# Performance work log

Measured on AMD Instinct MI355X. Metric: run time of the kernel, lower is better.

## Reference

```python
import jax, jax.numpy as jnp
import numpy as np
from jax import lax

DN = ('NCHW', 'OIHW', 'NCHW')


def squash(x):
    # x: [..., d]; squared-norm over last dim
    sq = jnp.sum(x * x, axis=-1, keepdims=True)
    return sq * x / ((1.0 + sq) * jnp.sqrt(sq))


def setup_inputs() -> dict:
    key = jax.random.key(0)
    ks = jax.random.split(key, 6)
    B = 512
    x = jax.random.normal(ks[0], (B, 1, 28, 28), dtype=jnp.float32)
    conv1_w = jax.random.normal(ks[1], (256, 1, 9, 9), dtype=jnp.float32) * 0.05
    conv1_b = jnp.zeros((256,), dtype=jnp.float32)
    conv2_w = jax.random.normal(ks[2], (256, 256, 9, 9), dtype=jnp.float32) * 0.02
    conv2_b = jnp.zeros((256,), dtype=jnp.float32)
    # W: [num_routes=1152, num_capsules=10, out_channels=16, in_channels=8]
    W = jax.random.normal(ks[3], (1152, 10, 16, 8), dtype=jnp.float32)
    return {"x": x, "conv1_w": conv1_w, "conv1_b": conv1_b,
            "conv2_w": conv2_w, "conv2_b": conv2_b, "W": W}


def reference(x, conv1_w, conv1_b, conv2_w, conv2_b, W):
    B = x.shape[0]
    # conv1 + ReLU: [B,1,28,28] -> [B,256,20,20]
    h = lax.conv_general_dilated(x, conv1_w, (1, 1), 'VALID', dimension_numbers=DN)
    h = jax.nn.relu(h + conv1_b[None, :, None, None])
    # primary capsule conv: [B,256,20,20] -> [B,256,6,6], stride 2
    h = lax.conv_general_dilated(h, conv2_w, (2, 2), 'VALID', dimension_numbers=DN)
    h = h + conv2_b[None, :, None, None]
    # reshape to capsules [B, 1152, 8] (matches torch .view on NCHW) and squash
    u = squash(h.reshape(B, -1, 8))
    # u_hat[b,r,c,o] = W[r,c,o,i] @ u[b,r,i]
    u_hat = jnp.einsum('rcoi,bri->brco', W, u)  # [B,1152,10,16]
    R, C = W.shape[0], W.shape[1]
    b_ij = jnp.zeros((R, C), dtype=x.dtype)
    num_iterations = 3
    for it in range(num_iterations):
        c_ij = jax.nn.softmax(b_ij, axis=0)          # softmax over routes
        s_j = jnp.einsum('rc,brco->bco', c_ij, u_hat)  # [B,10,16]
        v_j = squash(s_j)
        if it < num_iterations - 1:
            a_ij = jnp.einsum('brco,bco->brc', u_hat, v_j)  # agreement
            b_ij = b_ij + a_ij.mean(axis=0)
    return v_j  # [B,10,16]
```

## Files before the change

### kernel.cpp

```cpp
#include <hip/hip_runtime.h>
#include <stdint.h>


typedef unsigned short u16;
typedef unsigned int u32;
typedef _Float16 half8 __attribute__((ext_vector_type(8)));
typedef float f32x4 __attribute__((ext_vector_type(4)));

__device__ __forceinline__ u16 f2h(float f) {
  union { _Float16 h; u16 u; } cv;
  cv.h = (_Float16)f;
  return cv.u;
}

__device__ __forceinline__ void gload_lds16(const void* g, void* l) {
  __builtin_amdgcn_global_load_lds(
      (const __attribute__((address_space(1))) void*)g,
      (__attribute__((address_space(3))) void*)l, 16, 0, 0);
}

__global__ __launch_bounds__(256) void prologue_kernel(
    const float* __restrict__ x, const float* __restrict__ w1,
    const float* __restrict__ b1, const float* __restrict__ w2,
    const float* __restrict__ b2, u16* __restrict__ hT,
    u16* __restrict__ A2, float* __restrict__ u) {
  __shared__ __align__(16) char smraw[81 * 264 * 2];
  int bid = blockIdx.x;
  int tid = threadIdx.x;
  if (bid < 512) {
    float* xs = (float*)smraw;
    int b = bid;
    int co = tid;
    for (int i = co; i < 784; i += 256) xs[i] = x[(size_t)b * 784 + i];
    float w[81];
    const float* wp = w1 + co * 81;
#pragma unroll
    for (int k = 0; k < 81; ++k) w[k] = wp[k];
    float bias = b1[co];
    __syncthreads();
    u16* hb = hT + (size_t)b * 102400 + co;
    for (int yp = 0; yp < 10; ++yp) {
      int y0 = yp * 2;
      for (int g = 0; g < 5; ++g) {
        int xo = g * 4;
        float a0[4], a1[4];
#pragma unroll
        for (int j = 0; j < 4; ++j) { a0[j] = bias; a1[j] = bias; }
#pragma unroll
        for (int ky2 = 0; ky2 < 10; ++ky2) {
          const float* row = &xs[(y0 + ky2) * 28 + xo];
          float4 r0 = *(const float4*)row;
          float4 r1 = *(const float4*)(row + 4);
          float4 r2 = *(const float4*)(row + 8);
          float xr[12] = {r0.x, r0.y, r0.z, r0.w, r1.x, r1.y, r1.z, r1.w,
                          r2.x, r2.y, r2.z, r2.w};
          if (ky2 < 9) {
#pragma unroll
            for (int kx = 0; kx < 9; ++kx) {
              float wv = w[ky2 * 9 + kx];
              a0[0] = fmaf(wv, xr[kx], a0[0]);
              a0[1] = fmaf(wv, xr[kx + 1], a0[1]);
              a0[2] = fmaf(wv, xr[kx + 2], a0[2]);
              a0[3] = fmaf(wv, xr[kx + 3], a0[3]);
            }
          }
          if (ky2 >= 1) {
#pragma unroll
            for (int kx = 0; kx < 9; ++kx) {
              float wv = w[(ky2 - 1) * 9 + kx];
              a1[0] = fmaf(wv, xr[kx], a1[0]);
              a1[1] = fmaf(wv, xr[kx + 1], a1[1]);
              a1[2] = fmaf(wv, xr[kx + 2], a1[2]);
              a1[3] = fmaf(wv, xr[kx + 3], a1[3]);
            }
          }
        }
#pragma unroll
        for (int j = 0; j < 4; ++j) {
          hb[(y0 * 20 + xo + j) * 256] = f2h(fmaxf(a0[j], 0.f));
          hb[((y0 + 1) * 20 + xo + j) * 256] = f2h(fmaxf(a1[j], 0.f));
        }
      }
    }
  } else if (bid < 768) {
    u16* tl = (u16*)smraw;
    int co = bid - 512;
    const float* wp = w2 + (size_t)co * 20736;
#pragma unroll
    for (int k = 0; k < 81; ++k) {
      int li = k * 256 + tid;
      int ci = li / 81, t = li - ci * 81;
      tl[t * 264 + ci] = f2h(wp[li]);
    }
    __syncthreads();
    u16* op = A2 + (size_t)co * 20736;
    for (int oc = tid; oc < 2592; oc += 256) {
      int k0 = oc * 8;
      int t = k0 >> 8, ci0 = k0 & 255;
      *(uint4*)(op + k0) = *(const uint4*)&tl[t * 264 + ci0];
    }
  } else {
    int i = (bid - 768) * 256 + tid;
    int b = i / 2304, j0 = (i - b * 2304) * 4;
    float4 v;
    v.x = b2[j0 / 36]; v.y = b2[(j0 + 1) / 36];
    v.z = b2[(j0 + 2) / 36]; v.w = b2[(j0 + 3) / 36];
    *(float4*)(u + (size_t)b * 9216 + j0) = v;
  }
}

__global__ __launch_bounds__(512, 2) void conv2_kernel(
    const u16* __restrict__ hT, const u16* __restrict__ A2,
    float* __restrict__ u) {
  __shared__ __align__(16) u16 lds_[65536];
  char* const ldsc = (char*)lds_;
  const int bx = blockIdx.x;
  const int nbk = bx % 72, kz = bx / 72;
  const int n0 = nbk * 256;
  const int tid = threadIdx.x;
  const int lane = tid & 63, w = tid >> 6;
  const int wr = w >> 2, wc = w & 3;
  const int fr = lane & 15, fg = lane >> 4;
  const int w1024 = w * 1024;

  const int rA = tid >> 3;
  const int qsrc = (tid & 7) ^ (rA & 7);
  const int AbaseT = rA * 20736 + qsrc * 8;
  int Bb[4];
#pragma unroll
  for (int rg = 0; rg < 4; ++rg) {
    int n = n0 + rg * 64 + rA;
    int b = n / 36, sp = n - b * 36, oh = sp / 6, ow = sp - oh * 6;
    Bb[rg] = (b * 400 + oh * 40 + ow * 2) * 256 + qsrc * 8;
  }

  const int kx0 = (fg ^ (fr & 7)) << 4;
  const int kx1 = ((4 + fg) ^ (fr & 7)) << 4;
  const int wr16384 = wr * 16384;
  const int bh16384 = 32768 + (wc >> 1) * 16384;
  const int brow0 = (wc & 1) * 64;

  f32x4 acc[8][4] = {};
  half8 areg[4][2], breg[2][2];

#define STAGE_A(E, H, GT) do {                                               \
    char* p_ = ldsc + (E) * 65536 + (H) * 16384 + w1024;                     \
    gload_lds16(A2 + AbaseT + ((H) * 2 + 0) * 1327104 + (GT) * 64, p_);      \
    gload_lds16(A2 + AbaseT + ((H) * 2 + 1) * 1327104 + (GT) * 64, p_ + 8192); \
  } while (0)
#define STAGE_B(E, H, BOFF) do {                                             \
    char* p_ = ldsc + (E) * 65536 + 32768 + (H) * 16384 + w1024;             \
    gload_lds16(hT + Bb[(H) * 2 + 0] + (BOFF), p_);                          \
    gload_lds16(hT + Bb[(H) * 2 + 1] + (BOFF), p_ + 8192);                   \
  } while (0)
#define STAGE_ALL(E, GT) do {                                                \
    int tap_ = (GT) >> 2;                                                    \
    int kh_ = tap_ / 9, kw_ = tap_ - kh_ * 9;                                \
    int bo_ = (kh_ * 20 + kw_) * 256 + ((GT) & 3) * 64;                      \
    STAGE_A(E, 0, GT); STAGE_B(E, 0, bo_);                                   \
    STAGE_B(E, 1, bo_); STAGE_A(E, 1, GT);                                   \
  } while (0)
#define RD_A(D, MH) do { _Pragma("unroll")                                   \
    for (int mr = 0; mr < 4; ++mr) {                                         \
      const char* r_ = ldsc + (D) * 65536 + wr16384 +                        \
                       ((MH) * 64 + mr * 16 + fr) * 128;                     \
      areg[mr][0] = *(const half8*)(r_ + kx0);                               \
      areg[mr][1] = *(const half8*)(r_ + kx1);                               \
    } } while (0)
#define RD_B(D, NH) do { _Pragma("unroll")                                   \
    for (int nr = 0; nr < 2; ++nr) {                                         \
      const char* r_ = ldsc + (D) * 65536 + bh16384 +                        \
                       (brow0 + (NH) * 32 + nr * 16 + fr) * 128;             \
      breg[nr][0] = *(const half8*)(r_ + kx0);                               \
      breg[nr][1] = *(const half8*)(r_ + kx1);                               \
    } } while (0)
#define MM16(MH, NH) do {                                                    \
    __builtin_amdgcn_s_setprio(1);                                           \
    _Pragma("unroll") for (int mr = 0; mr < 4; ++mr)                         \
    _Pragma("unroll") for (int nr = 0; nr < 2; ++nr) {                       \
      acc[(MH)*4+mr][(NH)*2+nr] = __builtin_amdgcn_mfma_f32_16x16x32_f16(    \
          areg[mr][0], breg[nr][0], acc[(MH)*4+mr][(NH)*2+nr], 0, 0, 0);     \
      acc[(MH)*4+mr][(NH)*2+nr] = __builtin_amdgcn_mfma_f32_16x16x32_f16(    \
          areg[mr][1], breg[nr][1], acc[(MH)*4+mr][(NH)*2+nr], 0, 0, 0);     \
    }                                                                        \
    __builtin_amdgcn_s_setprio(0);                                           \
  } while (0)
#define BAR_PRE() do {                                                       \
    __builtin_amdgcn_s_barrier();                                            \
    asm volatile("s_waitcnt lgkmcnt(0)" ::: "memory");                       \
    __builtin_amdgcn_sched_barrier(0);                                       \
  } while (0)
#define BAR_ONLY() do {                                                      \
    __builtin_amdgcn_s_barrier();                                            \
    asm volatile("" ::: "memory");                                           \
  } while (0)
#define VM_BAR(N) do {                                                       \
    asm volatile("s_waitcnt vmcnt(" N ")" ::: "memory");                     \
    __builtin_amdgcn_s_barrier();                                            \
    asm volatile("" ::: "memory");                                           \
  } while (0)
#define TILE_STD(T, D, E) do {                                               \
    RD_A(D, 0); RD_B(D, 0);                                                  \
    STAGE_ALL(E, kz * 108 + (T) + 1);                                        \
    BAR_PRE(); MM16(0, 0); BAR_ONLY();                                       \
    RD_B(D, 1);                                                              \
    BAR_PRE(); MM16(0, 1); VM_BAR("8");                                      \
    RD_A(D, 1);                                                              \
    BAR_PRE(); MM16(1, 1); BAR_ONLY();                                       \
    RD_B(D, 0);                                                              \
    BAR_PRE(); MM16(1, 0); VM_BAR("2");                                      \
  } while (0)
#define TILE_LAST(D) do {                                                    \
    RD_A(D, 0); RD_B(D, 0);                                                  \
    BAR_PRE(); MM16(0, 0); BAR_ONLY();                                       \
    RD_B(D, 1);                                                              \
    BAR_PRE(); MM16(0, 1); VM_BAR("0");                                      \
    RD_A(D, 1);                                                              \
    BAR_PRE(); MM16(1, 1); BAR_ONLY();                                       \
    RD_B(D, 0);                                                              \
    BAR_PRE(); MM16(1, 0);                                                   \
  } while (0)

  STAGE_ALL(0, kz * 108);
  asm volatile("s_waitcnt vmcnt(2)" ::: "memory");
  __builtin_amdgcn_s_barrier();
  asm volatile("" ::: "memory");

  for (int tt = 0; tt < 53; ++tt) {
    TILE_STD(2 * tt, 0, 1);
    TILE_STD(2 * tt + 1, 1, 0);
  }
  TILE_STD(106, 0, 1);
  TILE_LAST(1);

#pragma unroll
  for (int nf = 0; nf < 4; ++nf) {
    int cn = n0 + wc * 64 + nf * 16 + fr;
    int ob = cn / 36;
    int os = cn - ob * 36;
    float* op = u + (size_t)ob * 9216 + os;
#pragma unroll
    for (int mf = 0; mf < 8; ++mf) {
      int row0 = wr * 128 + mf * 16 + fg * 4;
#pragma unroll
      for (int qq = 0; qq < 4; ++qq)
        atomicAdd(op + (row0 + qq) * 36, acc[mf][nf][qq]);
    }
  }
#undef STAGE_A
#undef STAGE_B
#undef STAGE_ALL
#undef RD_A
#undef RD_B
#undef MM16
#undef BAR_PRE
#undef BAR_ONLY
#undef VM_BAR
#undef TILE_STD
#undef TILE_LAST
}

__global__ __launch_bounds__(256) void squash_kernel(
    float* __restrict__ u, u16* __restrict__ ub) {
  int idx = blockIdx.x * 256 + threadIdx.x;
  float* up = u + (size_t)idx * 8;
  float4 a = *(const float4*)up;
  float4 c = *(const float4*)(up + 4);
  float sq = a.x * a.x + a.y * a.y + a.z * a.z + a.w * a.w +
             c.x * c.x + c.y * c.y + c.z * c.z + c.w * c.w;
  float f = sqrtf(sq) / (1.0f + sq);
  a.x *= f; a.y *= f; a.z *= f; a.w *= f;
  c.x *= f; c.y *= f; c.z *= f; c.w *= f;
  *(float4*)up = a;
  *(float4*)(up + 4) = c;
  u16 o[8];
  o[0] = f2h(a.x); o[1] = f2h(a.y); o[2] = f2h(a.z); o[3] = f2h(a.w);
  o[4] = f2h(c.x); o[5] = f2h(c.y); o[6] = f2h(c.z); o[7] = f2h(c.w);
  *(uint4*)(ub + (size_t)idx * 8) = *(uint4*)o;
}

__global__ __launch_bounds__(256) void transp_kernel(
    const u16* __restrict__ ub, u16* __restrict__ ubT) {
  __shared__ u16 tl[64][72];
  int ri0 = blockIdx.x * 64, b0 = blockIdx.y * 64;
  int tid = threadIdx.x;
  int br = tid >> 2, cq = tid & 3;
  const u16* ip = ub + (size_t)(b0 + br) * 9216 + ri0 + cq * 16;
  uint4 v0 = *(const uint4*)ip;
  uint4 v1 = *(const uint4*)(ip + 8);
  *(uint4*)&tl[br][cq * 16] = v0;
  *(uint4*)&tl[br][cq * 16 + 8] = v1;
  __syncthreads();
  int rr = tid >> 2, cb = tid & 3;
  u16 o0[8], o1[8];
#pragma unroll
  for (int j = 0; j < 8; ++j) {
    o0[j] = tl[cb * 16 + j][rr];
    o1[j] = tl[cb * 16 + 8 + j][rr];
  }
  u16* opp = ubT + (size_t)(ri0 + rr) * 512 + b0 + cb * 16;
  *(uint4*)opp = *(uint4*)o0;
  *(uint4*)(opp + 8) = *(uint4*)o1;
}

__global__ __launch_bounds__(256) void softmax_c_kernel(
    const float* __restrict__ bij, float* __restrict__ cT) {
  int c = blockIdx.x;
  int tid = threadIdx.x;
  __shared__ float red[256];
  float mx = -1e30f;
  for (int r = tid; r < 1152; r += 256) mx = fmaxf(mx, bij[r * 10 + c]);
  red[tid] = mx;
  __syncthreads();
  for (int s = 128; s > 0; s >>= 1) {
    if (tid < s) red[tid] = fmaxf(red[tid], red[tid + s]);
    __syncthreads();
  }
  mx = red[0];
  __syncthreads();
  float sum = 0.f;
  for (int r = tid; r < 1152; r += 256) sum += expf(bij[r * 10 + c] - mx);
  red[tid] = sum;
  __syncthreads();
  for (int s = 128; s > 0; s >>= 1) {
    if (tid < s) red[tid] += red[tid + s];
    __syncthreads();
  }
  float inv = 1.0f / red[0];
  for (int r = tid; r < 1152; r += 256)
    cT[c * 1152 + r] = expf(bij[r * 10 + c] - mx) * inv;
}

__global__ __launch_bounds__(256) void gemm_s_kernel(
    const float* __restrict__ W, const float* __restrict__ cT,
    const u16* __restrict__ ub, float* __restrict__ s) {
  __shared__ __align__(16) u16 Asl[160 * 72];
  __shared__ __align__(16) u16 Bsl[64 * 72];
  int nb = blockIdx.x & 7, kzi = blockIdx.x >> 3;
  int n0 = nb * 64, k0 = kzi * 256;
  int tid = threadIdx.x;
  int lane = tid & 63, wave = tid >> 6;
  int fr = lane & 15, fg = lane >> 4;

  f32x4 acc[10] = {};
#pragma unroll
  for (int st = 0; st < 4; ++st) {
    int kb = k0 + st * 64;
    __syncthreads();
#pragma unroll
    for (int j = 0; j < 5; ++j) {
      int c5 = tid + j * 256;
      int row = c5 >> 3, qq = c5 & 7;
      int cls = row >> 4, o = row & 15;
      int r = (kb + qq * 8) >> 3;
      const float* wp = W + (size_t)r * 1280 + cls * 128 + o * 8;
      float4 w0 = *(const float4*)wp;
      float4 w1 = *(const float4*)(wp + 4);
      float cs = cT[cls * 1152 + r] * 512.0f;
      u16 ov[8];
      ov[0] = f2h(w0.x * cs); ov[1] = f2h(w0.y * cs);
      ov[2] = f2h(w0.z * cs); ov[3] = f2h(w0.w * cs);
      ov[4] = f2h(w1.x * cs); ov[5] = f2h(w1.y * cs);
      ov[6] = f2h(w1.z * cs); ov[7] = f2h(w1.w * cs);
      *(uint4*)((char*)Asl + row * 144 + qq * 16) = *(uint4*)ov;
    }
#pragma unroll
    for (int j = 0; j < 2; ++j) {
      int c2 = tid + j * 256;
      int row = c2 >> 3, qq = c2 & 7;
      *(uint4*)((char*)Bsl + row * 144 + qq * 16) =
          *(const uint4*)(ub + (size_t)(n0 + row) * 9216 + kb + qq * 8);
    }
    __syncthreads();
#pragma unroll
    for (int s2 = 0; s2 < 2; ++s2) {
      int xg = (s2 * 4 + fg) * 16;
      half8 bf0 = *(const half8*)((char*)Bsl + (wave * 16 + fr) * 144 + xg);
#pragma unroll
      for (int m = 0; m < 10; ++m) {
        half8 af = *(const half8*)((char*)Asl + (m * 16 + fr) * 144 + xg);
        acc[m] = __builtin_amdgcn_mfma_f32_16x16x32_f16(af, bf0, acc[m], 0, 0, 0);
      }
    }
  }
  int bcol = n0 + wave * 16 + fr;
#pragma unroll
  for (int m = 0; m < 10; ++m)
#pragma unroll
    for (int qq = 0; qq < 4; ++qq)
      atomicAdd(s + (m * 16 + fg * 4 + qq) * 512 + bcol, acc[m][qq]);
}

__global__ __launch_bounds__(256) void squash_v_kernel(
    float* __restrict__ s, u16* __restrict__ vb) {
  int idx = blockIdx.x * 256 + threadIdx.x;
  int c = idx >> 9, b = idx & 511;
  float vals[16];
  float sq = 0.f;
#pragma unroll
  for (int o = 0; o < 16; ++o) {
    float v = s[(c * 16 + o) * 512 + b] * (1.0f / 512.0f);
    vals[o] = v;
    sq += v * v;
  }
#pragma unroll
  for (int o = 0; o < 16; ++o) s[(c * 16 + o) * 512 + b] = 0.f;
  float f = sqrtf(sq) / (1.0f + sq);
#pragma unroll
  for (int o = 0; o < 16; ++o)
    vb[(c * 16 + o) * 512 + b] = f2h(vals[o] * f * 4096.0f);
}

__global__ __launch_bounds__(256) void gemm_gc_kernel(
    const u16* __restrict__ vb, const u16* __restrict__ ubT,
    const float* __restrict__ W, float* __restrict__ bij) {
  __shared__ __align__(16) u16 Agl[160 * 72];
  __shared__ __align__(16) u16 Bgl[128 * 72];
  __shared__ float Gl[160 * 129];
  int nb = blockIdx.x % 72, kzi = blockIdx.x / 72;
  int n0 = nb * 128, k0 = kzi * 128;
  int tid = threadIdx.x;
  int lane = tid & 63, wave = tid >> 6;
  int fr = lane & 15, fg = lane >> 4;
  f32x4 acc[10][2] = {};
#pragma unroll
  for (int st = 0; st < 2; ++st) {
    int kb = k0 + st * 64;
    __syncthreads();
#pragma unroll
    for (int j = 0; j < 5; ++j) {
      int c5 = tid + j * 256;
      int row = c5 >> 3, qq = c5 & 7;
      *(uint4*)((char*)Agl + row * 144 + qq * 16) =
          *(const uint4*)(vb + (size_t)row * 512 + kb + qq * 8);
    }
#pragma unroll
    for (int j = 0; j < 4; ++j) {
      int c4 = tid + j * 256;
      int row = c4 >> 3, qq = c4 & 7;
      *(uint4*)((char*)Bgl + row * 144 + qq * 16) =
          *(const uint4*)(ubT + (size_t)(n0 + row) * 512 + kb + qq * 8);
    }
    __syncthreads();
#pragma unroll
    for (int s2 = 0; s2 < 2; ++s2) {
      int xg = (s2 * 4 + fg) * 16;
      half8 bfv[2];
#pragma unroll
      for (int nn = 0; nn < 2; ++nn)
        bfv[nn] = *(const half8*)((char*)Bgl + (wave * 32 + nn * 16 + fr) * 144 + xg);
#pragma unroll
      for (int m = 0; m < 10; ++m) {
        half8 af = *(const half8*)((char*)Agl + (m * 16 + fr) * 144 + xg);
#pragma unroll
        for (int nn = 0; nn < 2; ++nn)
          acc[m][nn] = __builtin_amdgcn_mfma_f32_16x16x32_f16(af, bfv[nn],
                                                             acc[m][nn], 0, 0, 0);
      }
    }
  }
#pragma unroll
  for (int m = 0; m < 10; ++m)
#pragma unroll
    for (int nn = 0; nn < 2; ++nn) {
      int col = wave * 32 + nn * 16 + fr;
#pragma unroll
      for (int qq = 0; qq < 4; ++qq)
        Gl[(m * 16 + fg * 4 + qq) * 129 + col] = acc[m][nn][qq];
    }
  __syncthreads();
  if (tid < 160) {
    int rl = tid / 10, c = tid - rl * 10;
    int r = (n0 >> 3) + rl;
    const float* wp = W + (size_t)r * 1280 + c * 128;
    float a = 0.f;
#pragma unroll 4
    for (int o = 0; o < 16; ++o) {
      const float* gp = &Gl[(c * 16 + o) * 129 + rl * 8];
#pragma unroll
      for (int i = 0; i < 8; ++i) a = fmaf(wp[o * 8 + i], gp[i], a);
    }
    atomicAdd(&bij[r * 10 + c], a * (1.0f / (512.0f * 4096.0f)));
  }
}

__global__ __launch_bounds__(256) void route_final_kernel(
    const float* __restrict__ cT, const float* __restrict__ u,
    const float* __restrict__ W, float* __restrict__ outp) {
  int c = blockIdx.y, b0 = blockIdx.x * 16;
  int tid = threadIdx.x, lb = tid >> 4, o = tid & 15;
  __shared__ float us[16][32][8];
  __shared__ float Wl[32][128];
  __shared__ float cs[32];
  float acc = 0.f;
  for (int r0 = 0; r0 < 1152; r0 += 32) {
    __syncthreads();
#pragma unroll
    for (int j = 0; j < 4; ++j) {
      int i4 = tid + j * 256;
      int bb = i4 >> 6, rem = i4 & 63;
      int rr = rem >> 1, hf = rem & 1;
      *(float4*)&us[bb][rr][hf * 4] =
          *(const float4*)&u[(size_t)(b0 + bb) * 9216 + (r0 + rr) * 8 + hf * 4];
    }
#pragma unroll
    for (int j = 0; j < 4; ++j) {
      int i4 = tid + j * 256;
      int rw = i4 >> 5, c4 = i4 & 31;
      *(float4*)&Wl[rw][c4 * 4] =
          *(const float4*)&W[((size_t)(r0 + rw) * 10 + c) * 128 + c4 * 4];
    }
    if (tid < 32) cs[tid] = cT[c * 1152 + r0 + tid];
    __syncthreads();
#pragma unroll 4
    for (int rr = 0; rr < 32; ++rr) {
      float4 w0 = *(const float4*)&Wl[rr][o * 8];
      float4 w1v = *(const float4*)&Wl[rr][o * 8 + 4];
      float4 ua = *(const float4*)&us[lb][rr][0];
      float4 ub4 = *(const float4*)&us[lb][rr][4];
      float d = w0.x * ua.x + w0.y * ua.y + w0.z * ua.z + w0.w * ua.w +
                w1v.x * ub4.x + w1v.y * ub4.y + w1v.z * ub4.z + w1v.w * ub4.w;
      acc = fmaf(cs[rr], d, acc);
    }
  }
  float sq = acc * acc;
  sq += __shfl_xor(sq, 1, 64);
  sq += __shfl_xor(sq, 2, 64);
  sq += __shfl_xor(sq, 4, 64);
  sq += __shfl_xor(sq, 8, 64);
  float f = sqrtf(sq) / (1.0f + sq);
  outp[((size_t)(b0 + lb) * 10 + c) * 16 + o] = acc * f;
}

extern "C" void kernel_launch(void* const* d_in, const int* in_sizes, int n_in,
                              void* d_out, int out_size, void* d_ws, size_t ws_size,
                              hipStream_t stream) {
  const float* x  = (const float*)d_in[0];
  const float* w1 = (const float*)d_in[1];
  const float* b1 = (const float*)d_in[2];
  const float* w2 = (const float*)d_in[3];
  const float* b2 = (const float*)d_in[4];
  const float* W  = (const float*)d_in[5];
  char* ws = (char*)d_ws;
  u16*   hT  = (u16*)ws;
  u16*   A2  = (u16*)(ws + 104857600);
  float* u   = (float*)(ws + 115474432);
  float* bij = (float*)(ws + 134348800);
  float* cT  = (float*)(ws + 134394880);
  float* s   = (float*)(ws + 134440960);
  u16*   ub  = (u16*)ws;
  u16*   ubT = (u16*)(ws + 9437184);
  u16*   vb  = (u16*)(ws + 21823488);
  float* out = (float*)d_out;

  hipMemsetAsync(bij, 0, 46080, stream);
  hipMemsetAsync(s, 0, 327680, stream);
  prologue_kernel<<<5376, 256, 0, stream>>>(x, w1, b1, w2, b2, hT, A2, u);
  conv2_kernel<<<216, 512, 0, stream>>>(hT, A2, u);
  squash_kernel<<<2304, 256, 0, stream>>>(u, ub);
  transp_kernel<<<dim3(144, 8), 256, 0, stream>>>(ub, ubT);
  for (int it = 0; it < 3; ++it) {
    softmax_c_kernel<<<10, 256, 0, stream>>>(bij, cT);
    if (it < 2) {
      gemm_s_kernel<<<288, 256, 0, stream>>>(W, cT, ub, s);
      squash_v_kernel<<<20, 256, 0, stream>>>(s, vb);
      gemm_gc_kernel<<<288, 256, 0, stream>>>(vb, ubT, W, bij);
    } else {
      route_final_kernel<<<dim3(32, 10), 256, 0, stream>>>(cT, u, W, out);
    }
  }
}
```

Measured before the change: 642.5 us.

## Merge MFMA phases per tile and read W directly in final routing

The conv2 GEMM main loop is restructured from four barrier-separated MFMA phases per tile into two. Both B fragments are now held in registers at once (breg gains an NH dimension), and the A staging is split so half is issued early and half mid-tile. The LDS layout of the A stage changes, and vmcnt waits are adjusted to match. This removes two barriers per tile at the cost of more live registers. Separately, the final routing kernel drops its LDS staging of W and loads W rows straight from global memory inside the inner loop.

Result: faster. 621.9 us (-3.2%).

```diff
diff --git a/kernel.cpp b/kernel.cpp
--- a/kernel.cpp
+++ b/kernel.cpp
@@ -141,24 +141,18 @@
   const int brow0 = (wc & 1) * 64;
 
   f32x4 acc[8][4] = {};
-  half8 areg[4][2], breg[2][2];
+  half8 areg[4][2], breg[2][2][2];
 
 #define STAGE_A(E, H, GT) do {                                               \
-    char* p_ = ldsc + (E) * 65536 + (H) * 16384 + w1024;                     \
-    gload_lds16(A2 + AbaseT + ((H) * 2 + 0) * 1327104 + (GT) * 64, p_);      \
-    gload_lds16(A2 + AbaseT + ((H) * 2 + 1) * 1327104 + (GT) * 64, p_ + 8192); \
+    char* p0_ = ldsc + (E) * 65536 + (H) * 8192 + w1024;                     \
+    gload_lds16(A2 + AbaseT + (H) * 1327104 + (GT) * 64, p0_);               \
+    char* p1_ = ldsc + (E) * 65536 + 16384 + (H) * 8192 + w1024;             \
+    gload_lds16(A2 + AbaseT + (2 + (H)) * 1327104 + (GT) * 64, p1_);         \
   } while (0)
 #define STAGE_B(E, H, BOFF) do {                                             \
     char* p_ = ldsc + (E) * 65536 + 32768 + (H) * 16384 + w1024;             \
     gload_lds16(hT + Bb[(H) * 2 + 0] + (BOFF), p_);                          \
     gload_lds16(hT + Bb[(H) * 2 + 1] + (BOFF), p_ + 8192);                   \
-  } while (0)
-#define STAGE_ALL(E, GT) do {                                                \
-    int tap_ = (GT) >> 2;                                                    \
-    int kh_ = tap_ / 9, kw_ = tap_ - kh_ * 9;                                \
-    int bo_ = (kh_ * 20 + kw_) * 256 + ((GT) & 3) * 64;                      \
-    STAGE_A(E, 0, GT); STAGE_B(E, 0, bo_);                                   \
-    STAGE_B(E, 1, bo_); STAGE_A(E, 1, GT);                                   \
   } while (0)
 #define RD_A(D, MH) do { _Pragma("unroll")                                   \
     for (int mr = 0; mr < 4; ++mr) {                                         \
@@ -171,17 +165,17 @@
     for (int nr = 0; nr < 2; ++nr) {                                         \
       const char* r_ = ldsc + (D) * 65536 + bh16384 +                        \
                        (brow0 + (NH) * 32 + nr * 16 + fr) * 128;             \
-      breg[nr][0] = *(const half8*)(r_ + kx0);                               \
-      breg[nr][1] = *(const half8*)(r_ + kx1);                               \
+      breg[NH][nr][0] = *(const half8*)(r_ + kx0);                           \
+      breg[NH][nr][1] = *(const half8*)(r_ + kx1);                           \
     } } while (0)
 #define MM16(MH, NH) do {                                                    \
     __builtin_amdgcn_s_setprio(1);                                           \
     _Pragma("unroll") for (int mr = 0; mr < 4; ++mr)                         \
     _Pragma("unroll") for (int nr = 0; nr < 2; ++nr) {                       \
       acc[(MH)*4+mr][(NH)*2+nr] = __builtin_amdgcn_mfma_f32_16x16x32_f16(    \
-          areg[mr][0], breg[nr][0], acc[(MH)*4+mr][(NH)*2+nr], 0, 0, 0);     \
+          areg[mr][0], breg[NH][nr][0], acc[(MH)*4+mr][(NH)*2+nr], 0, 0, 0); \
       acc[(MH)*4+mr][(NH)*2+nr] = __builtin_amdgcn_mfma_f32_16x16x32_f16(    \
-          areg[mr][1], breg[nr][1], acc[(MH)*4+mr][(NH)*2+nr], 0, 0, 0);     \
+          areg[mr][1], breg[NH][nr][1], acc[(MH)*4+mr][(NH)*2+nr], 0, 0, 0); \
     }                                                                        \
     __builtin_amdgcn_s_setprio(0);                                           \
   } while (0)
@@ -190,48 +184,47 @@
     asm volatile("s_waitcnt lgkmcnt(0)" ::: "memory");                       \
     __builtin_amdgcn_sched_barrier(0);                                       \
   } while (0)
-#define BAR_ONLY() do {                                                      \
-    __builtin_amdgcn_s_barrier();                                            \
-    asm volatile("" ::: "memory");                                           \
-  } while (0)
 #define VM_BAR(N) do {                                                       \
     asm volatile("s_waitcnt vmcnt(" N ")" ::: "memory");                     \
     __builtin_amdgcn_s_barrier();                                            \
     asm volatile("" ::: "memory");                                           \
   } while (0)
-#define TILE_STD(T, D, E) do {                                               \
-    RD_A(D, 0); RD_B(D, 0);                                                  \
-    STAGE_ALL(E, kz * 108 + (T) + 1);                                        \
-    BAR_PRE(); MM16(0, 0); BAR_ONLY();                                       \
-    RD_B(D, 1);                                                              \
-    BAR_PRE(); MM16(0, 1); VM_BAR("8");                                      \
+#define TILE_STD2(T, D, E) do {                                              \
+    const int gt_ = kz * 108 + (T) + 1;                                      \
+    int tap_ = gt_ >> 2;                                                     \
+    int kh_ = tap_ / 9, kw_ = tap_ - kh_ * 9;                                \
+    int bo_ = (kh_ * 20 + kw_) * 256 + (gt_ & 3) * 64;                       \
+    RD_A(D, 0); RD_B(D, 0); RD_B(D, 1);                                      \
+    STAGE_A(E, 0, gt_); STAGE_B(E, 0, bo_); STAGE_B(E, 1, bo_);              \
+    BAR_PRE(); MM16(0, 0); MM16(0, 1); VM_BAR("6");                          \
     RD_A(D, 1);                                                              \
-    BAR_PRE(); MM16(1, 1); BAR_ONLY();                                       \
-    RD_B(D, 0);                                                              \
-    BAR_PRE(); MM16(1, 0); VM_BAR("2");                                      \
-  } while (0)
-#define TILE_LAST(D) do {                                                    \
-    RD_A(D, 0); RD_B(D, 0);                                                  \
-    BAR_PRE(); MM16(0, 0); BAR_ONLY();                                       \
-    RD_B(D, 1);                                                              \
-    BAR_PRE(); MM16(0, 1); VM_BAR("0");                                      \
+    STAGE_A(E, 1, gt_);                                                      \
+    BAR_PRE(); MM16(1, 0); MM16(1, 1); VM_BAR("2");                          \
+  } while (0)
+#define TILE_LAST2(D) do {                                                   \
+    RD_A(D, 0); RD_B(D, 0); RD_B(D, 1);                                      \
+    BAR_PRE(); MM16(0, 0); MM16(0, 1); VM_BAR("0");                          \
     RD_A(D, 1);                                                              \
-    BAR_PRE(); MM16(1, 1); BAR_ONLY();                                       \
-    RD_B(D, 0);                                                              \
-    BAR_PRE(); MM16(1, 0);                                                   \
-  } while (0)
-
-  STAGE_ALL(0, kz * 108);
-  asm volatile("s_waitcnt vmcnt(2)" ::: "memory");
-  __builtin_amdgcn_s_barrier();
-  asm volatile("" ::: "memory");
-
+    BAR_PRE(); MM16(1, 0); MM16(1, 1);                                       \
+  } while (0)
+
+  {
+    const int gt0 = kz * 108;
+    int tap = gt0 >> 2;
+    int kh = tap / 9, kw = tap - kh * 9;
+    int bo0 = (kh * 20 + kw) * 256 + (gt0 & 3) * 64;
+    STAGE_A(0, 0, gt0); STAGE_B(0, 0, bo0); STAGE_B(0, 1, bo0);
+    STAGE_A(0, 1, gt0);
+    asm volatile("s_waitcnt vmcnt(2)" ::: "memory");
+    __builtin_amdgcn_s_barrier();
+    asm volatile("" ::: "memory");
+  }
   for (int tt = 0; tt < 53; ++tt) {
-    TILE_STD(2 * tt, 0, 1);
-    TILE_STD(2 * tt + 1, 1, 0);
-  }
-  TILE_STD(106, 0, 1);
-  TILE_LAST(1);
+    TILE_STD2(2 * tt, 0, 1);
+    TILE_STD2(2 * tt + 1, 1, 0);
+  }
+  TILE_STD2(106, 0, 1);
+  TILE_LAST2(1);
 
 #pragma unroll
   for (int nf = 0; nf < 4; ++nf) {
@@ -249,15 +242,13 @@
   }
 #undef STAGE_A
 #undef STAGE_B
-#undef STAGE_ALL
 #undef RD_A
 #undef RD_B
 #undef MM16
 #undef BAR_PRE
-#undef BAR_ONLY
 #undef VM_BAR
-#undef TILE_STD
-#undef TILE_LAST
+#undef TILE_STD2
+#undef TILE_LAST2
 }
 
 __global__ __launch_bounds__(256) void squash_kernel(
@@ -490,7 +481,6 @@
   int c = blockIdx.y, b0 = blockIdx.x * 16;
   int tid = threadIdx.x, lb = tid >> 4, o = tid & 15;
   __shared__ float us[16][32][8];
-  __shared__ float Wl[32][128];
   __shared__ float cs[32];
   float acc = 0.f;
   for (int r0 = 0; r0 < 1152; r0 += 32) {
@@ -503,19 +493,13 @@
       *(float4*)&us[bb][rr][hf * 4] =
           *(const float4*)&u[(size_t)(b0 + bb) * 9216 + (r0 + rr) * 8 + hf * 4];
     }
-#pragma unroll
-    for (int j = 0; j < 4; ++j) {
-      int i4 = tid + j * 256;
-      int rw = i4 >> 5, c4 = i4 & 31;
-      *(float4*)&Wl[rw][c4 * 4] =
-          *(const float4*)&W[((size_t)(r0 + rw) * 10 + c) * 128 + c4 * 4];
-    }
     if (tid < 32) cs[tid] = cT[c * 1152 + r0 + tid];
     __syncthreads();
 #pragma unroll 4
     for (int rr = 0; rr < 32; ++rr) {
-      float4 w0 = *(const float4*)&Wl[rr][o * 8];
-      float4 w1v = *(const float4*)&Wl[rr][o * 8 + 4];
+      const float* wp = W + ((size_t)(r0 + rr) * 10 + c) * 128 + o * 8;
+      float4 w0 = *(const float4*)wp;
+      float4 w1v = *(const float4*)(wp + 4);
       float4 ua = *(const float4*)&us[lb][rr][0];
       float4 ub4 = *(const float4*)&us[lb][rr][4];
       float d = w0.x * ua.x + w0.y * ua.y + w0.z * ua.z + w0.w * ua.w +
```
